# Kernel tuning notes

Measured on AMD Instinct MI355X. Metric: run time of the kernel, lower is better.

## Reference

```python
import jax, jax.numpy as jnp
import numpy as np


def setup_inputs() -> dict:
    key = jax.random.key(0)
    ks = jax.random.split(key, 4)
    B, M, D = 512, 40, 64
    # split_half=True with layers [200,200,200]: prev = 40 -> 100 -> 100
    x = jax.random.normal(ks[0], (B, M, D), dtype=jnp.float32)
    w1 = jax.random.normal(ks[1], (200, M * 40), dtype=jnp.float32) * 0.02
    w2 = jax.random.normal(ks[2], (200, M * 100), dtype=jnp.float32) * 0.02
    w3 = jax.random.normal(ks[3], (200, M * 100), dtype=jnp.float32) * 0.02
    b1 = jnp.zeros((200,), dtype=jnp.float32)
    b2 = jnp.zeros((200,), dtype=jnp.float32)
    b3 = jnp.zeros((200,), dtype=jnp.float32)
    return {"x": x, "w1": w1, "b1": b1, "w2": w2, "b2": b2, "w3": w3, "b3": b3}


def reference(x, w1, b1, w2, b2, w3, b3):
    B, M, D = x.shape
    params = [(w1, b1), (w2, b2), (w3, b3)]
    n_layers = len(params)
    hidden = x  # (B, prev, D), starts as x0
    outs = []
    for i, (w, b) in enumerate(params):
        # outer product over field dims, flattened channel-major as in torch .view
        outer = jnp.einsum('bmd,bnd->bmnd', x, hidden).reshape(B, -1, D)
        # Conv1d kernel_size=1 == per-position linear over channels
        out = jax.nn.relu(jnp.einsum('bcd,oc->bod', outer, w) + b[None, :, None])
        if i < n_layers - 1:  # split_half
            half = out.shape[1] // 2
            out, direct = out[:, :half, :], out[:, half:, :]
            outs.append(direct)
        else:
            outs.append(out)
        hidden = out
    return jnp.concatenate(outs, axis=1).sum(axis=2)  # (B, 100+100+200)
```

## Files before the change

### kernel.cpp

```cpp
#include <hip/hip_runtime.h>
#include <hip/hip_bf16.h>


typedef float f32x4 __attribute__((ext_vector_type(4)));
typedef short bf16x8 __attribute__((ext_vector_type(8)));
typedef unsigned int uint;

#define XS_STR 44
#define HS_STR 108

struct LDSState {
    __hip_bfloat16 xs[2][64][XS_STR];
    __hip_bfloat16 hs[2][2][64][HS_STR];
    uint U[4][2][64][16];
    float psum[2][2][208];
};

static __device__ __forceinline__ float bflo(uint u) {
    uint v = u << 16; return __builtin_bit_cast(float, v);
}
static __device__ __forceinline__ float bfhi(uint u) {
    uint v = u & 0xffff0000u; return __builtin_bit_cast(float, v);
}
static __device__ __forceinline__ uint pk_bf16(float a, float b) {
    uint r; asm("v_cvt_pk_bf16_f32 %0, %1, %2" : "=v"(r) : "v"(a), "v"(b));
    return r;
}

#define PHASE_BAR() do {                                   \
    asm volatile("s_waitcnt lgkmcnt(0)" ::: "memory");     \
    __builtin_amdgcn_sched_barrier(0);                     \
    __builtin_amdgcn_s_barrier();                          \
    __builtin_amdgcn_sched_barrier(0);                     \
} while (0)

template<int DIV, int NK, int HASH, int ROWLO, int ROWOFF, int HSTRIDE, int A>
__device__ __forceinline__ void layer_core(
    LDSState* L, const bf16x8* __restrict__ wpk, const float* __restrict__ bias,
    const __hip_bfloat16* __restrict__ h0, const __hip_bfloat16* __restrict__ h1,
    int dstpp, int lp, float* __restrict__ outb, int tid, int mt0)
{
    const int lane = tid & 63;
    const int wv = tid >> 6;
    const int wn = (wv >> 1) & 1, nh = wv & 1;
    const int q = lane >> 4, lr = lane & 15, d = lane;

    const int hdr = (lr >> 1) & 7;
    const uint* ub  = &L->U[0][0][0][0] + wn * 1024;
    const uint* roA = ub + (lr * 16 + 2 * ((2 * q) ^ hdr));
    const uint* roB = ub + (lr * 16 + 2 * ((2 * q + 1) ^ hdr));

    const int hdw = (d >> 1) & 7;
    uint* wb = &L->U[0][0][d][0] + 2 * ((wv >> 1) ^ hdw) + (wv & 1);

    const __hip_bfloat16* xb0 = &L->xs[0][d][0];
    const __hip_bfloat16* xb1 = &L->xs[1][d][0];
    const __hip_bfloat16* hb0 = h0 + d * HSTRIDE;
    const __hip_bfloat16* hb1 = h1 + d * HSTRIDE;

    f32x4 acc[A][2];
    #pragma unroll
    for (int mi = 0; mi < A; ++mi) {
        acc[mi][0] = {0.f, 0.f, 0.f, 0.f};
        acc[mi][1] = {0.f, 0.f, 0.f, 0.f};
    }

    int bm = 0, bn = 2 * wv, bk = 0;
    auto build = [&](int slab_dw) {
        if (bk < NK) {
            float xf0 = __bfloat162float(xb0[bm]);
            float xf1 = __bfloat162float(xb1[bm]);
            uint ha = *(const uint*)(hb0 + bn);
            uint hc = *(const uint*)(hb1 + bn);
            wb[slab_dw]        = pk_bf16(xf0 * bflo(ha), xf0 * bfhi(ha));
            wb[slab_dw + 1024] = pk_bf16(xf1 * bflo(hc), xf1 * bfhi(hc));
            bn += 32;
            if (bn >= DIV) { bn -= DIV; ++bm; }
            ++bk;
        }
    };

    auto consume = [&](int slab_dw, bf16x8* f) {
        bf16x8 bv[2];
        #pragma unroll
        for (int j = 0; j < 2; ++j) {
            const int nj = 2 * nh + j;
            union { uint2 u2[2]; bf16x8 v; } t;
            t.u2[0] = *(const uint2*)(roA + slab_dw + nj * 256);
            t.u2[1] = *(const uint2*)(roB + slab_dw + nj * 256);
            bv[j] = t.v;
        }
        #pragma unroll
        for (int mi = 0; mi < A; ++mi) {
            acc[mi][0] = __builtin_amdgcn_mfma_f32_16x16x32_bf16(
                f[mi], bv[0], acc[mi][0], 0, 0, 0);
            acc[mi][1] = __builtin_amdgcn_mfma_f32_16x16x32_bf16(
                f[mi], bv[1], acc[mi][1], 0, 0, 0);
        }
    };

    const bf16x8* pw = wpk + (size_t)mt0 * NK * 64 + lane;
    bf16x8 fA[A], fB[A];
    #pragma unroll
    for (int mi = 0; mi < A; ++mi) {
        fA[mi] = pw[(size_t)mi * NK * 64];
        fB[mi] = pw[(size_t)mi * NK * 64 + 64];
    }
    build(0);
    build(2048);
    __syncthreads();

    #pragma unroll 1
    for (int s = 0; s + 2 <= NK; s += 2) {
        const int sd0 = (s & 3) * 2048;
        const int sd1 = ((s + 1) & 3) * 2048;
        const int sd2 = ((s + 2) & 3) * 2048;
        const int sd3 = ((s + 3) & 3) * 2048;
        consume(sd0, fA);
        if (s + 2 < NK) {
            #pragma unroll
            for (int mi = 0; mi < A; ++mi)
                fA[mi] = pw[(size_t)mi * NK * 64 + (size_t)(s + 2) * 64];
        }
        consume(sd1, fB);
        if (s + 3 < NK) {
            #pragma unroll
            for (int mi = 0; mi < A; ++mi)
                fB[mi] = pw[(size_t)mi * NK * 64 + (size_t)(s + 3) * 64];
        }
        build(sd2);
        build(sd3);
        PHASE_BAR();
    }
    if (NK & 1) consume(0, fA);

    const int d0 = 32 * nh + lr, d1 = d0 + 16;
    #pragma unroll
    for (int mi = 0; mi < A; ++mi) {
        const int ob = 16 * (mt0 + mi) + 4 * q;
        #pragma unroll
        for (int reg = 0; reg < 4; ++reg) {
            const int o = ob + reg;
            if (o < 200) {
                const float bs = bias[o];
                float r0 = fmaxf(acc[mi][0][reg] + bs, 0.f);
                float r1 = fmaxf(acc[mi][1][reg] + bs, 0.f);
                if (HASH && o < 100) {
                    L->hs[dstpp][wn][d0][o] = __float2bfloat16(r0);
                    L->hs[dstpp][wn][d1][o] = __float2bfloat16(r1);
                }
                if (nh == 0 && o >= ROWLO) {
                    float sv = r0 + r1;
                    sv += __shfl_xor(sv, 1, 64);
                    sv += __shfl_xor(sv, 2, 64);
                    sv += __shfl_xor(sv, 4, 64);
                    sv += __shfl_xor(sv, 8, 64);
                    if (lr == 0) L->psum[lp][wn][o] = sv;
                }
            }
        }
    }
    __syncthreads();
    if (nh == 1) {
        #pragma unroll
        for (int mi = 0; mi < A; ++mi) {
            const int ob = 16 * (mt0 + mi) + 4 * q;
            #pragma unroll
            for (int reg = 0; reg < 4; ++reg) {
                const int o = ob + reg;
                if (o < 200 && o >= ROWLO) {
                    const float bs = bias[o];
                    float r0 = fmaxf(acc[mi][0][reg] + bs, 0.f);
                    float r1 = fmaxf(acc[mi][1][reg] + bs, 0.f);
                    float sv = r0 + r1;
                    sv += __shfl_xor(sv, 1, 64);
                    sv += __shfl_xor(sv, 2, 64);
                    sv += __shfl_xor(sv, 4, 64);
                    sv += __shfl_xor(sv, 8, 64);
                    if (lr == 0)
                        outb[ROWOFF + (o - ROWLO)] = sv + L->psum[lp][wn][o];
                }
            }
        }
    }
}

template<int A>
__device__ __forceinline__ void run_layers(
    LDSState* L, const bf16x8* w1p, const bf16x8* w2p, const bf16x8* w3p,
    const float* b1, const float* b2, const float* b3,
    float* outb, int tid, int mt0)
{
    layer_core< 40,  50, 1, 100,   0, XS_STR, A>(L, w1p, b1,
        &L->xs[0][0][0], &L->xs[1][0][0], 0, 0, outb, tid, mt0);
    layer_core<100, 125, 1, 100, 100, HS_STR, A>(L, w2p, b2,
        &L->hs[0][0][0][0], &L->hs[0][1][0][0], 1, 1, outb, tid, mt0);
    layer_core<100, 125, 0,   0, 200, HS_STR, A>(L, w3p, b3,
        &L->hs[1][0][0][0], &L->hs[1][1][0][0], 0, 0, outb, tid, mt0);
}

__global__ __launch_bounds__(1024)
void fused_mfma(const float* __restrict__ x,
                const bf16x8* __restrict__ wpk,
                const float* __restrict__ b1, const float* __restrict__ b2,
                const float* __restrict__ b3, float* __restrict__ out) {
    __shared__ LDSState L;
    const int tid = threadIdx.x;
    const int bi  = blockIdx.x;

    const float* xg = x + (size_t)(2 * bi) * 2560;
    for (int i = tid; i < 5120; i += 1024) {
        int bb = (i >= 2560) ? 1 : 0;
        int r  = i - bb * 2560;
        L.xs[bb][r & 63][r >> 6] = __float2bfloat16(xg[(size_t)bb * 2560 + r]);
    }
    __syncthreads();

    const int wn = (tid >> 7) & 1;
    float* outb = out + (size_t)(2 * bi + wn) * 400;

    const bf16x8* w1p = wpk;
    const bf16x8* w2p = wpk + 41600;
    const bf16x8* w3p = wpk + 145600;

    const int gm = tid >> 8;
    if (gm == 0)
        run_layers<4>(&L, w1p, w2p, w3p, b1, b2, b3, outb, tid, 0);
    else
        run_layers<3>(&L, w1p, w2p, w3p, b1, b2, b3, outb, tid, 4 + 3 * (gm - 1));
}

__global__ void convert_pack(const float* __restrict__ w1, const float* __restrict__ w2,
                             const float* __restrict__ w3, uint4* __restrict__ outp) {
    int c = blockIdx.x * 256 + threadIdx.x;
    if (c >= 249600) return;
    const float* src; int K, base;
    if (c < 41600)       { src = w1; K = 1600; base = c; }
    else if (c < 145600) { src = w2; K = 4000; base = c - 41600; }
    else                 { src = w3; K = 4000; base = c - 145600; }
    const int NS   = K / 32;
    const int lane = base & 63;
    const int t    = base >> 6;
    const int mt   = t / NS;
    const int s    = t - mt * NS;
    const int row  = 16 * mt + (lane & 15);
    const int k0   = 32 * s + 8 * (lane >> 4);
    uint o[4];
    if (row < 200) {
        const float* p = src + (size_t)row * K + k0;
        #pragma unroll
        for (int j = 0; j < 4; ++j) {
            __hip_bfloat16 lo = __float2bfloat16(p[2 * j]);
            __hip_bfloat16 hi = __float2bfloat16(p[2 * j + 1]);
            o[j] = (uint)__builtin_bit_cast(unsigned short, lo)
                 | ((uint)__builtin_bit_cast(unsigned short, hi) << 16);
        }
    } else {
        #pragma unroll
        for (int j = 0; j < 4; ++j) o[j] = 0u;
    }
    uint4 v; v.x = o[0]; v.y = o[1]; v.z = o[2]; v.w = o[3];
    outp[c] = v;
}

__global__ __launch_bounds__(512, 1)
void fused_bilinear_kernel(const float* __restrict__ x,
                           const float* __restrict__ w1, const float* __restrict__ b1,
                           const float* __restrict__ w2, const float* __restrict__ b2,
                           const float* __restrict__ w3, const float* __restrict__ b3,
                           float* __restrict__ out) {
    const int b   = blockIdx.x;
    const int tid = threadIdx.x;
    const int d   = tid & 63;
    const int wv  = tid >> 6;

    __shared__ float xs[40][64];
    __shared__ float hs[100][64];

    const float* xb = x + (size_t)b * 40 * 64;
    for (int i = tid; i < 40 * 64; i += 512) ((float*)xs)[i] = xb[i];
    __syncthreads();

    float xr[40];
    #pragma unroll
    for (int m = 0; m < 40; ++m) xr[m] = xs[m][d];
    float hr[100];
    const int o0 = __builtin_amdgcn_readfirstlane(wv * 25);

    for (int oi = 0; oi < 25; ++oi) {
        const int o = o0 + oi;
        const float* __restrict__ wrow = w1 + (size_t)o * 1600;
        float s = b1[o];
        for (int m = 0; m < 40; ++m) {
            const float* __restrict__ wm = wrow + m * 40;
            float a0 = 0.f, a1 = 0.f, a2 = 0.f, a3 = 0.f;
            #pragma unroll
            for (int n = 0; n < 40; n += 4) {
                a0 = fmaf(wm[n + 0], xr[n + 0], a0);
                a1 = fmaf(wm[n + 1], xr[n + 1], a1);
                a2 = fmaf(wm[n + 2], xr[n + 2], a2);
                a3 = fmaf(wm[n + 3], xr[n + 3], a3);
            }
            s = fmaf(xs[m][d], (a0 + a1) + (a2 + a3), s);
        }
        s = fmaxf(s, 0.f);
        if (o < 100) hs[o][d] = s;
        else {
            float r = s;
            #pragma unroll
            for (int off = 32; off > 0; off >>= 1) r += __shfl_xor(r, off, 64);
            if (d == 0) out[(size_t)b * 400 + (o - 100)] = r;
        }
    }
    __syncthreads();
    #pragma unroll
    for (int n = 0; n < 100; ++n) hr[n] = hs[n][d];
    __syncthreads();

    for (int oi = 0; oi < 25; ++oi) {
        const int o = o0 + oi;
        const float* __restrict__ wrow = w2 + (size_t)o * 4000;
        float s = b2[o];
        for (int m = 0; m < 40; ++m) {
            const float* __restrict__ wm = wrow + m * 100;
            float a0 = 0.f, a1 = 0.f, a2 = 0.f, a3 = 0.f;
            #pragma unroll
            for (int n = 0; n < 100; n += 4) {
                a0 = fmaf(wm[n + 0], hr[n + 0], a0);
                a1 = fmaf(wm[n + 1], hr[n + 1], a1);
                a2 = fmaf(wm[n + 2], hr[n + 2], a2);
                a3 = fmaf(wm[n + 3], hr[n + 3], a3);
            }
            s = fmaf(xs[m][d], (a0 + a1) + (a2 + a3), s);
        }
        s = fmaxf(s, 0.f);
        if (o < 100) hs[o][d] = s;
        else {
            float r = s;
            #pragma unroll
            for (int off = 32; off > 0; off >>= 1) r += __shfl_xor(r, off, 64);
            if (d == 0) out[(size_t)b * 400 + 100 + (o - 100)] = r;
        }
    }
    __syncthreads();
    #pragma unroll
    for (int n = 0; n < 100; ++n) hr[n] = hs[n][d];

    for (int oi = 0; oi < 25; ++oi) {
        const int o = o0 + oi;
        const float* __restrict__ wrow = w3 + (size_t)o * 4000;
        float s = b3[o];
        for (int m = 0; m < 40; ++m) {
            const float* __restrict__ wm = wrow + m * 100;
            float a0 = 0.f, a1 = 0.f, a2 = 0.f, a3 = 0.f;
            #pragma unroll
            for (int n = 0; n < 100; n += 4) {
                a0 = fmaf(wm[n + 0], hr[n + 0], a0);
                a1 = fmaf(wm[n + 1], hr[n + 1], a1);
                a2 = fmaf(wm[n + 2], hr[n + 2], a2);
                a3 = fmaf(wm[n + 3], hr[n + 3], a3);
            }
            s = fmaf(xs[m][d], (a0 + a1) + (a2 + a3), s);
        }
        s = fmaxf(s, 0.f);
        float r = s;
        #pragma unroll
        for (int off = 32; off > 0; off >>= 1) r += __shfl_xor(r, off, 64);
        if (d == 0) out[(size_t)b * 400 + 200 + o] = r;
    }
}

extern "C" void kernel_launch(void* const* d_in, const int* in_sizes, int n_in,
                              void* d_out, int out_size, void* d_ws, size_t ws_size,
                              hipStream_t stream) {
    const float* x  = (const float*)d_in[0];
    const float* w1 = (const float*)d_in[1];
    const float* b1 = (const float*)d_in[2];
    const float* w2 = (const float*)d_in[3];
    const float* b2 = (const float*)d_in[4];
    const float* w3 = (const float*)d_in[5];
    const float* b3 = (const float*)d_in[6];
    float* out = (float*)d_out;

    if (ws_size >= 249600u * 16u) {
        uint4* wp = (uint4*)d_ws;
        convert_pack<<<dim3(975), dim3(256), 0, stream>>>(w1, w2, w3, wp);
        fused_mfma<<<dim3(256), dim3(1024), 0, stream>>>(
            x, (const bf16x8*)wp, b1, b2, b3, out);
    } else {
        fused_bilinear_kernel<<<dim3(512), dim3(512), 0, stream>>>(
            x, w1, b1, w2, b2, w3, b3, out);
    }
}
```

Measured before the change: 195.6 us.

## Process one batch element per 512-thread block instead of two per 1024-thread block

```diff
diff --git a/kernel.cpp b/kernel.cpp
--- a/kernel.cpp
+++ b/kernel.cpp
@@ -10,10 +10,10 @@
 #define HS_STR 108
 
 struct LDSState {
-    __hip_bfloat16 xs[2][64][XS_STR];
-    __hip_bfloat16 hs[2][2][64][HS_STR];
-    uint U[4][2][64][16];
-    float psum[2][2][208];
+    __hip_bfloat16 xs[64][44];
+    __hip_bfloat16 hs[2][64][108];
+    uint U[4][64][16];
+    float psum[304];
 };
 
 static __device__ __forceinline__ float bflo(uint u) {
@@ -37,26 +37,24 @@
 template<int DIV, int NK, int HASH, int ROWLO, int ROWOFF, int HSTRIDE, int A>
 __device__ __forceinline__ void layer_core(
     LDSState* L, const bf16x8* __restrict__ wpk, const float* __restrict__ bias,
-    const __hip_bfloat16* __restrict__ h0, const __hip_bfloat16* __restrict__ h1,
-    int dstpp, int lp, float* __restrict__ outb, int tid, int mt0)
+    const __hip_bfloat16* __restrict__ hbase,
+    int dstpp, int psoff, float* __restrict__ outb, int tid, int mt0)
 {
     const int lane = tid & 63;
     const int wv = tid >> 6;
-    const int wn = (wv >> 1) & 1, nh = wv & 1;
+    const int nh = wv & 1;
     const int q = lane >> 4, lr = lane & 15, d = lane;
 
     const int hdr = (lr >> 1) & 7;
-    const uint* ub  = &L->U[0][0][0][0] + wn * 1024;
+    const uint* ub  = &L->U[0][0][0];
     const uint* roA = ub + (lr * 16 + 2 * ((2 * q) ^ hdr));
     const uint* roB = ub + (lr * 16 + 2 * ((2 * q + 1) ^ hdr));
 
     const int hdw = (d >> 1) & 7;
-    uint* wb = &L->U[0][0][d][0] + 2 * ((wv >> 1) ^ hdw) + (wv & 1);
-
-    const __hip_bfloat16* xb0 = &L->xs[0][d][0];
-    const __hip_bfloat16* xb1 = &L->xs[1][d][0];
-    const __hip_bfloat16* hb0 = h0 + d * HSTRIDE;
-    const __hip_bfloat16* hb1 = h1 + d * HSTRIDE;
+    uint* wb = &L->U[0][d][0] + 2 * (wv ^ hdw);
+
+    const __hip_bfloat16* xrow = &L->xs[d][0];
+    const __hip_bfloat16* hrow = hbase + d * HSTRIDE;
 
     f32x4 acc[A][2];
     #pragma unroll
@@ -65,15 +63,17 @@
         acc[mi][1] = {0.f, 0.f, 0.f, 0.f};
     }
 
-    int bm = 0, bn = 2 * wv, bk = 0;
+    int bm = (4 * wv) / DIV;
+    int bn = 4 * wv;
+    int bk = 0;
     auto build = [&](int slab_dw) {
         if (bk < NK) {
-            float xf0 = __bfloat162float(xb0[bm]);
-            float xf1 = __bfloat162float(xb1[bm]);
-            uint ha = *(const uint*)(hb0 + bn);
-            uint hc = *(const uint*)(hb1 + bn);
-            wb[slab_dw]        = pk_bf16(xf0 * bflo(ha), xf0 * bfhi(ha));
-            wb[slab_dw + 1024] = pk_bf16(xf1 * bflo(hc), xf1 * bfhi(hc));
+            float xf = __bfloat162float(xrow[bm]);
+            uint2 ha = *(const uint2*)(hrow + bn);
+            uint2 w;
+            w.x = pk_bf16(xf * bflo(ha.x), xf * bfhi(ha.x));
+            w.y = pk_bf16(xf * bflo(ha.y), xf * bfhi(ha.y));
+            *(uint2*)(wb + slab_dw) = w;
             bn += 32;
             if (bn >= DIV) { bn -= DIV; ++bm; }
             ++bk;
@@ -107,15 +107,15 @@
         fB[mi] = pw[(size_t)mi * NK * 64 + 64];
     }
     build(0);
-    build(2048);
+    build(1024);
     __syncthreads();
 
     #pragma unroll 1
     for (int s = 0; s + 2 <= NK; s += 2) {
-        const int sd0 = (s & 3) * 2048;
-        const int sd1 = ((s + 1) & 3) * 2048;
-        const int sd2 = ((s + 2) & 3) * 2048;
-        const int sd3 = ((s + 3) & 3) * 2048;
+        const int sd0 = (s & 3) * 1024;
+        const int sd1 = ((s + 1) & 3) * 1024;
+        const int sd2 = ((s + 2) & 3) * 1024;
+        const int sd3 = ((s + 3) & 3) * 1024;
         consume(sd0, fA);
         if (s + 2 < NK) {
             #pragma unroll
@@ -146,8 +146,8 @@
                 float r0 = fmaxf(acc[mi][0][reg] + bs, 0.f);
                 float r1 = fmaxf(acc[mi][1][reg] + bs, 0.f);
                 if (HASH && o < 100) {
-                    L->hs[dstpp][wn][d0][o] = __float2bfloat16(r0);
-                    L->hs[dstpp][wn][d1][o] = __float2bfloat16(r1);
+                    L->hs[dstpp][d0][o] = __float2bfloat16(r0);
+                    L->hs[dstpp][d1][o] = __float2bfloat16(r1);
                 }
                 if (nh == 0 && o >= ROWLO) {
                     float sv = r0 + r1;
@@ -155,7 +155,7 @@
                     sv += __shfl_xor(sv, 2, 64);
                     sv += __shfl_xor(sv, 4, 64);
                     sv += __shfl_xor(sv, 8, 64);
-                    if (lr == 0) L->psum[lp][wn][o] = sv;
+                    if (lr == 0) L->psum[psoff + (o - ROWLO)] = sv;
                 }
             }
         }
@@ -178,7 +178,8 @@
                     sv += __shfl_xor(sv, 4, 64);
                     sv += __shfl_xor(sv, 8, 64);
                     if (lr == 0)
-                        outb[ROWOFF + (o - ROWLO)] = sv + L->psum[lp][wn][o];
+                        outb[ROWOFF + (o - ROWLO)] =
+                            sv + L->psum[psoff + (o - ROWLO)];
                 }
             }
         }
@@ -192,14 +193,14 @@
     float* outb, int tid, int mt0)
 {
     layer_core< 40,  50, 1, 100,   0, XS_STR, A>(L, w1p, b1,
-        &L->xs[0][0][0], &L->xs[1][0][0], 0, 0, outb, tid, mt0);
+        &L->xs[0][0],    0,   0, outb, tid, mt0);
     layer_core<100, 125, 1, 100, 100, HS_STR, A>(L, w2p, b2,
-        &L->hs[0][0][0][0], &L->hs[0][1][0][0], 1, 1, outb, tid, mt0);
+        &L->hs[0][0][0], 1, 200, outb, tid, mt0);
     layer_core<100, 125, 0,   0, 200, HS_STR, A>(L, w3p, b3,
-        &L->hs[1][0][0][0], &L->hs[1][1][0][0], 0, 0, outb, tid, mt0);
-}
-
-__global__ __launch_bounds__(1024)
+        &L->hs[1][0][0], 0,   0, outb, tid, mt0);
+}
+
+__global__ __launch_bounds__(512, 4)
 void fused_mfma(const float* __restrict__ x,
                 const bf16x8* __restrict__ wpk,
                 const float* __restrict__ b1, const float* __restrict__ b2,
@@ -208,22 +209,19 @@
     const int tid = threadIdx.x;
     const int bi  = blockIdx.x;
 
-    const float* xg = x + (size_t)(2 * bi) * 2560;
-    for (int i = tid; i < 5120; i += 1024) {
-        int bb = (i >= 2560) ? 1 : 0;
-        int r  = i - bb * 2560;
-        L.xs[bb][r & 63][r >> 6] = __float2bfloat16(xg[(size_t)bb * 2560 + r]);
-    }
-    __syncthreads();
-
-    const int wn = (tid >> 7) & 1;
-    float* outb = out + (size_t)(2 * bi + wn) * 400;
+    const float* xg = x + (size_t)bi * 2560;
+    for (int i = tid; i < 2560; i += 512) {
+        L.xs[i & 63][i >> 6] = __float2bfloat16(xg[i]);
+    }
+    __syncthreads();
+
+    float* outb = out + (size_t)bi * 400;
 
     const bf16x8* w1p = wpk;
     const bf16x8* w2p = wpk + 41600;
     const bf16x8* w3p = wpk + 145600;
 
-    const int gm = tid >> 8;
+    const int gm = (tid >> 7);
     if (gm == 0)
         run_layers<4>(&L, w1p, w2p, w3p, b1, b2, b3, outb, tid, 0);
     else
@@ -385,7 +383,7 @@
     if (ws_size >= 249600u * 16u) {
         uint4* wp = (uint4*)d_ws;
         convert_pack<<<dim3(975), dim3(256), 0, stream>>>(w1, w2, w3, wp);
-        fused_mfma<<<dim3(256), dim3(1024), 0, stream>>>(
+        fused_mfma<<<dim3(512), dim3(512), 0, stream>>>(
             x, (const bf16x8*)wp, b1, b2, b3, out);
     } else {
         fused_bilinear_kernel<<<dim3(512), dim3(512), 0, stream>>>(
```

Measured after the change: 184.2 us. -5.8%, faster.
